# Optimization experiments

Measured on AMD Instinct MI355X. Metric: run time of the kernel, lower is better.

The kernel has to match this reference:

```python
import jax, jax.numpy as jnp
import numpy as np

B, N, D = 16, 2048, 4        # batch, input points, input feature dim (x,y,e1,e2)
G = 45                        # folding grid side -> M = G*G = 2025 output points
M = G * G
CW = 512                      # codeword dim
H1, H2 = 64, 128              # encoder hidden dims
FH = 512                      # folding MLP hidden dim


def _glorot(key, shape):
    fan_in, fan_out = shape[0], shape[1]
    s = jnp.sqrt(2.0 / (fan_in + fan_out)).astype(jnp.float32)
    return jax.random.normal(key, shape, dtype=jnp.float32) * s


def setup_inputs() -> dict:
    key = jax.random.key(0)
    ks = jax.random.split(key, 16)
    inp = {
        "points": jax.random.normal(ks[0], (B, N, D), dtype=jnp.float32),
        # encoder shared MLP: D -> H1 -> H2 -> CW, max-pool over N
        "ew1": _glorot(ks[1], (D, H1)),  "eb1": jnp.zeros((H1,), jnp.float32),
        "ew2": _glorot(ks[2], (H1, H2)), "eb2": jnp.zeros((H2,), jnp.float32),
        "ew3": _glorot(ks[3], (H2, CW)), "eb3": jnp.zeros((CW,), jnp.float32),
        # folding decoder
        "f1w1": _glorot(ks[4], (CW + 2, FH)), "f1b1": jnp.zeros((FH,), jnp.float32),
        "f1w2": _glorot(ks[5], (FH, FH)),     "f1b2": jnp.zeros((FH,), jnp.float32),
        "f1w3": _glorot(ks[6], (FH, 3)),      "f1b3": jnp.zeros((3,), jnp.float32),
        "f2w1": _glorot(ks[7], (CW + 3, FH)), "f2b1": jnp.zeros((FH,), jnp.float32),
        "f2w2": _glorot(ks[8], (FH, FH)),     "f2b2": jnp.zeros((FH,), jnp.float32),
        "f2w3": _glorot(ks[9], (FH, 3)),      "f2b3": jnp.zeros((3,), jnp.float32),
    }
    # fixed 2D folding grid in [-0.3, 0.3]^2, (M, 2)
    lin = jnp.linspace(-0.3, 0.3, G, dtype=jnp.float32)
    gx, gy = jnp.meshgrid(lin, lin, indexing="ij")
    inp["grid"] = jnp.stack([gx.ravel(), gy.ravel()], axis=-1)
    return inp


def _encode(points, ew1, eb1, ew2, eb2, ew3, eb3):
    h = jax.nn.relu(points @ ew1 + eb1)     # (B, N, H1)
    h = jax.nn.relu(h @ ew2 + eb2)          # (B, N, H2)
    h = h @ ew3 + eb3                       # (B, N, CW)
    return jnp.max(h, axis=1)               # (B, CW) codeword theta


def _decode(theta, grid, f1w1, f1b1, f1w2, f1b2, f1w3, f1b3,
            f2w1, f2b1, f2w2, f2b2, f2w3, f2b3):
    th = jnp.broadcast_to(theta[:, None, :], (theta.shape[0], M, CW))
    g = jnp.broadcast_to(grid[None], (theta.shape[0], M, 2))
    # folding 1: (codeword, 2D grid) -> 3D
    x = jnp.concatenate([th, g], axis=-1)
    x = jax.nn.relu(x @ f1w1 + f1b1)
    x = jax.nn.relu(x @ f1w2 + f1b2)
    fold1 = x @ f1w3 + f1b3                 # (B, M, 3)
    # folding 2: (codeword, intermediate 3D) -> 3D
    x = jnp.concatenate([th, fold1], axis=-1)
    x = jax.nn.relu(x @ f2w1 + f2b1)
    x = jax.nn.relu(x @ f2w2 + f2b2)
    return x @ f2w3 + f2b3                  # (B, M, 3)


def _chamfer(a, b):
    # a: (B, N, 3), b: (B, M, 3); squared-distance chamfer, both directions
    a2 = jnp.sum(a * a, axis=-1)                          # (B, N)
    b2 = jnp.sum(b * b, axis=-1)                          # (B, M)
    ab = jnp.einsum("bnd,bmd->bnm", a, b)                  # (B, N, M)
    d2 = a2[:, :, None] + b2[:, None, :] - 2.0 * ab
    d2 = jnp.maximum(d2, 0.0)
    return jnp.mean(jnp.min(d2, axis=2)) + jnp.mean(jnp.min(d2, axis=1))


def reference(points, ew1, eb1, ew2, eb2, ew3, eb3, grid,
              f1w1, f1b1, f1w2, f1b2, f1w3, f1b3,
              f2w1, f2b1, f2w2, f2b2, f2w3, f2b3):
    theta = _encode(points, ew1, eb1, ew2, eb2, ew3, eb3)
    pc_out = _decode(theta, grid, f1w1, f1b1, f1w2, f1b2, f1w3, f1b3,
                     f2w1, f2b1, f2w2, f2b2, f2w3, f2b3)
    # pc_input: (x, y, sum of energy channels)  -> (B, N, 3)
    energy = jnp.sum(points[:, :, 2:], axis=-1, keepdims=True)
    pc_input = jnp.concatenate([points[:, :, :2], energy], axis=-1)
    loss = _chamfer(pc_input, pc_out)
    return theta, pc_out, loss
```

## Files before the change

kernel.cpp:

```cpp
#include <hip/hip_runtime.h>

#define NBATCH 16
#define NPTS   2048
#define MQ     2025
#define CWDIM  512
#define NROWS  32400

typedef __attribute__((ext_vector_type(8))) short bf16x8;
typedef __attribute__((ext_vector_type(4))) float f32x4;

__device__ __forceinline__ unsigned fkey(float f) {
  unsigned u = __float_as_uint(f);
  return (u & 0x80000000u) ? ~u : (u | 0x80000000u);
}
__device__ __forceinline__ float funkey(unsigned u) {
  unsigned v = (u & 0x80000000u) ? (u ^ 0x80000000u) : ~u;
  return __uint_as_float(v);
}
__device__ __forceinline__ unsigned short f2bf(float f) {
  unsigned u = __float_as_uint(f);
  u = (u + 0x7FFFu + ((u >> 16) & 1u)) >> 16;
  return (unsigned short)u;
}

__global__ __launch_bounds__(256) void tconv_kernel(
    const float* __restrict__ ew2, unsigned short* __restrict__ ew2T)
{
  __shared__ float tile[32][33];
  const int tidx = blockIdx.x;
  const int kt = tidx >> 2, nt = tidx & 3;
  const int tx = threadIdx.x & 31, ty = threadIdx.x >> 5;
  #pragma unroll
  for (int j = 0; j < 4; ++j)
    tile[ty + 8 * j][tx] = ew2[(size_t)(kt * 32 + ty + 8 * j) * 128 + nt * 32 + tx];
  __syncthreads();
  #pragma unroll
  for (int j = 0; j < 4; ++j)
    ew2T[(size_t)(nt * 32 + ty + 8 * j) * 64 + kt * 32 + tx] = f2bf(tile[tx][ty + 8 * j]);
}

__global__ __launch_bounds__(256) void w2chunk_kernel(
    const float* __restrict__ f1w2, const float* __restrict__ f2w2,
    unsigned short* __restrict__ w2C)
{
  const int gid = blockIdx.x * 256 + threadIdx.x;
  const int s = gid >> 15;
  const int rem = gid & 32767;
  const int c16 = rem & 15, hi = (rem >> 4) & 3, cblk = (rem >> 6) & 31, kt = rem >> 11;
  const int col = cblk * 16 + c16;
  const float* src = s ? f2w2 : f1w2;
  unsigned short tmp[8];
  #pragma unroll
  for (int j = 0; j < 8; ++j)
    tmp[j] = f2bf(src[(size_t)(kt * 32 + hi * 8 + j) * 512 + col]);
  int4 pk;
  pk.x = (int)((unsigned)tmp[0] | ((unsigned)tmp[1] << 16));
  pk.y = (int)((unsigned)tmp[2] | ((unsigned)tmp[3] << 16));
  pk.z = (int)((unsigned)tmp[4] | ((unsigned)tmp[5] << 16));
  pk.w = (int)((unsigned)tmp[6] | ((unsigned)tmp[7] << 16));
  *(int4*)&w2C[(size_t)s * 262144 + (size_t)rem * 8] = pk;
}

__global__ __launch_bounds__(256) void ew3chunk_kernel(
    const float* __restrict__ ew3, unsigned short* __restrict__ ew3C)
{
  const int gid = blockIdx.x * 256 + threadIdx.x;
  const int c16 = gid & 15, hi = (gid >> 4) & 3, cblk = (gid >> 6) & 31, kblk = gid >> 11;
  const int col = cblk * 16 + c16;
  unsigned short tmp[8];
  #pragma unroll
  for (int j = 0; j < 8; ++j)
    tmp[j] = f2bf(ew3[(size_t)(kblk * 32 + hi * 8 + j) * 512 + col]);
  int4 pk;
  pk.x = (int)((unsigned)tmp[0] | ((unsigned)tmp[1] << 16));
  pk.y = (int)((unsigned)tmp[2] | ((unsigned)tmp[3] << 16));
  pk.z = (int)((unsigned)tmp[4] | ((unsigned)tmp[5] << 16));
  pk.w = (int)((unsigned)tmp[6] | ((unsigned)tmp[7] << 16));
  *(int4*)&ew3C[(size_t)gid * 8] = pk;
}

__global__ __launch_bounds__(512, 2) void enc2_kernel(
    const float* __restrict__ pts,
    const float* __restrict__ ew1, const float* __restrict__ eb1,
    const unsigned short* __restrict__ ew2T, const float* __restrict__ eb2,
    const unsigned short* __restrict__ ew3C, const float* __restrict__ eb3,
    unsigned* __restrict__ keys)
{
  __shared__ unsigned short h1s[64 * 64];
  __shared__ unsigned short h2s[64 * 128];
  __shared__ float s_pts[64][4];
  const int t = threadIdx.x;
  const int b = blockIdx.x >> 5, p0 = (blockIdx.x & 31) << 6;
  if (t < 64)
    *(float4*)&s_pts[t][0] = *(const float4*)(pts + ((size_t)b * NPTS + p0 + t) * 4);
  __syncthreads();

  {
    const int c = t & 63;
    const float w0 = ew1[c], w1 = ew1[64 + c], w2 = ew1[128 + c], w3 = ew1[192 + c];
    const float bb = eb1[c];
    #pragma unroll
    for (int i = 0; i < 8; ++i) {
      const int p = i * 8 + (t >> 6);
      float acc = bb + s_pts[p][0] * w0 + s_pts[p][1] * w1 + s_pts[p][2] * w2 + s_pts[p][3] * w3;
      unsigned byte = ((unsigned)p << 7) + ((unsigned)c << 1);
      byte ^= ((unsigned)(p & 7)) << 4;
      h1s[byte >> 1] = f2bf(fmaxf(acc, 0.f));
    }
  }
  __syncthreads();

  const int wv = t >> 6, lane = t & 63, l15 = lane & 15, hi = lane >> 4;

  {
    f32x4 acc[4];
    #pragma unroll
    for (int m = 0; m < 4; ++m) acc[m] = (f32x4){0.f, 0.f, 0.f, 0.f};
    const int col = 16 * wv + l15;
    #pragma unroll
    for (int kk = 0; kk < 64; kk += 32) {
      bf16x8 bv = *(const bf16x8*)(ew2T + (size_t)col * 64 + kk + hi * 8);
      #pragma unroll
      for (int m = 0; m < 4; ++m) {
        const int row = 16 * m + l15;
        unsigned byte = ((unsigned)row << 7) + ((unsigned)((kk + hi * 8)) << 1);
        byte ^= ((unsigned)(row & 7)) << 4;
        bf16x8 av = *(const bf16x8*)&h1s[byte >> 1];
        acc[m] = __builtin_amdgcn_mfma_f32_16x16x32_bf16(av, bv, acc[m], 0, 0, 0);
      }
    }
    const float b2c = eb2[col];
    #pragma unroll
    for (int m = 0; m < 4; ++m)
      #pragma unroll
      for (int r = 0; r < 4; ++r) {
        const int row = 16 * m + hi * 4 + r;
        unsigned byte = ((unsigned)row << 8) + ((unsigned)col << 1);
        byte ^= ((unsigned)(row & 7)) << 4;
        h2s[byte >> 1] = f2bf(fmaxf(acc[m][r] + b2c, 0.f));
      }
  }
  __syncthreads();

  {
    f32x4 acc[4][4];
    #pragma unroll
    for (int m = 0; m < 4; ++m)
      #pragma unroll
      for (int n = 0; n < 4; ++n) acc[m][n] = (f32x4){0.f, 0.f, 0.f, 0.f};
    #pragma unroll
    for (int kk = 0; kk < 128; kk += 32) {
      bf16x8 av[4];
      #pragma unroll
      for (int m = 0; m < 4; ++m) {
        const int row = 16 * m + l15;
        unsigned byte = ((unsigned)row << 8) + ((unsigned)(kk + hi * 8) << 1);
        byte ^= ((unsigned)(row & 7)) << 4;
        av[m] = *(const bf16x8*)&h2s[byte >> 1];
      }
      #pragma unroll
      for (int n = 0; n < 4; ++n) {
        bf16x8 bv = *(const bf16x8*)(ew3C +
            (size_t)(((kk >> 5) * 32 + 4 * wv + n) * 512) + lane * 8);
        #pragma unroll
        for (int m = 0; m < 4; ++m)
          acc[m][n] = __builtin_amdgcn_mfma_f32_16x16x32_bf16(av[m], bv, acc[m][n], 0, 0, 0);
      }
    }
    #pragma unroll
    for (int n = 0; n < 4; ++n) {
      const int col = 64 * wv + 16 * n + l15;
      float mx = -1e30f;
      #pragma unroll
      for (int m = 0; m < 4; ++m)
        #pragma unroll
        for (int r = 0; r < 4; ++r) mx = fmaxf(mx, acc[m][n][r]);
      mx = fmaxf(mx, __shfl_xor(mx, 16));
      mx = fmaxf(mx, __shfl_xor(mx, 32));
      if (hi == 0) atomicMax(&keys[b * CWDIM + col], fkey(mx + eb3[col]));
    }
  }
}

__global__ __launch_bounds__(256) void decode_kernel(const unsigned* __restrict__ keys,
                                                     float* __restrict__ theta) {
  int i = blockIdx.x * 256 + threadIdx.x;
  theta[i] = funkey(keys[i]);
}

__global__ __launch_bounds__(256) void h1base_kernel(
    const float* __restrict__ theta,
    const float* __restrict__ f1w1, const float* __restrict__ f1b1,
    const float* __restrict__ f2w1, const float* __restrict__ f2b1,
    float* __restrict__ h1b)
{
  int gid = blockIdx.x * 256 + threadIdx.x;
  int half = gid >> 14;
  int rem = gid & 16383;
  int stage = rem >> 13, bb = (rem >> 9) & 15, c = rem & 511;
  const float* w = stage ? f2w1 : f1w1;
  float acc = 0.f;
  if (half == 0) acc = stage ? f2b1[c] : f1b1[c];
  const float* th = theta + bb * 512 + half * 256;
  const float* wp = w + (size_t)(half * 256) * 512 + c;
  #pragma unroll 8
  for (int k = 0; k < 256; ++k) acc += th[k] * wp[(size_t)k * 512];
  atomicAdd(&h1b[rem], acc);
}

struct Fold5Smem {
  unsigned short sA[64 * 512];
  float red[8][32][3];
  float ext[64][4];
  int   rowbb[64];
};

template <int ST>
__device__ __forceinline__ void fold5_stage(Fold5Smem& S, int t, int r0,
    const float* __restrict__ h1bg,
    const float* __restrict__ w1,
    const unsigned short* __restrict__ wst,
    const float* __restrict__ b2, const float* __restrict__ w3,
    const float* __restrict__ b3, float* __restrict__ out_pc)
{
  constexpr int NE = ST ? 3 : 2;
  const int wv = t >> 6, lane = t & 63, l15 = lane & 15, hi = lane >> 4;
  const int wm = wv >> 2, wn = wv & 3;

  __syncthreads();

  {
    const int row = t & 63;
    const int bb = S.rowbb[row];
    const float e0 = S.ext[row][0], e1 = S.ext[row][1];
    float e2 = 0.f;
    if (NE == 3) e2 = S.ext[row][2];
    const float* hb  = h1bg + ST * 8192 + bb * 512;
    const float* wr0 = w1 + (size_t)512 * 512;
    const float* wr1 = wr0 + 512;
    const float* wr2 = wr1 + 512;
    #pragma unroll
    for (int i = 0; i < 8; ++i) {
      const int ko = (t >> 6) * 8 + i;
      const int c0 = ko * 8;
      float v[8];
      #pragma unroll
      for (int hf = 0; hf < 2; ++hf) {
        float4 h = *(const float4*)(hb + c0 + hf * 4);
        float4 a = *(const float4*)(wr0 + c0 + hf * 4);
        float4 bq = *(const float4*)(wr1 + c0 + hf * 4);
        v[hf * 4 + 0] = h.x + e0 * a.x + e1 * bq.x;
        v[hf * 4 + 1] = h.y + e0 * a.y + e1 * bq.y;
        v[hf * 4 + 2] = h.z + e0 * a.z + e1 * bq.z;
        v[hf * 4 + 3] = h.w + e0 * a.w + e1 * bq.w;
        if (NE == 3) {
          float4 cq = *(const float4*)(wr2 + c0 + hf * 4);
          v[hf * 4 + 0] += e2 * cq.x; v[hf * 4 + 1] += e2 * cq.y;
          v[hf * 4 + 2] += e2 * cq.z; v[hf * 4 + 3] += e2 * cq.w;
        }
      }
      int4 pk;
      pk.x = (int)((unsigned)f2bf(fmaxf(v[0], 0.f)) | ((unsigned)f2bf(fmaxf(v[1], 0.f)) << 16));
      pk.y = (int)((unsigned)f2bf(fmaxf(v[2], 0.f)) | ((unsigned)f2bf(fmaxf(v[3], 0.f)) << 16));
      pk.z = (int)((unsigned)f2bf(fmaxf(v[4], 0.f)) | ((unsigned)f2bf(fmaxf(v[5], 0.f)) << 16));
      pk.w = (int)((unsigned)f2bf(fmaxf(v[6], 0.f)) | ((unsigned)f2bf(fmaxf(v[7], 0.f)) << 16));
      *(int4*)&S.sA[(unsigned)(((ko >> 2) * 4 + (row >> 4)) * 512 + (ko & 3) * 128 + (row & 15) * 8)] = pk;
    }
  }
  __syncthreads();

  float p[2][4][3];
  #pragma unroll
  for (int m = 0; m < 2; ++m)
    #pragma unroll
    for (int r = 0; r < 4; ++r)
      #pragma unroll
      for (int jj = 0; jj < 3; ++jj) p[m][r][jj] = 0.f;

  #pragma unroll 1
  for (int pass = 0; pass < 2; ++pass) {
    f32x4 acc[2][4];
    #pragma unroll
    for (int m = 0; m < 2; ++m)
      #pragma unroll
      for (int n = 0; n < 4; ++n) acc[m][n] = (f32x4){0.f, 0.f, 0.f, 0.f};

    const unsigned short* wb = wst + (size_t)(pass * 16 + wn * 4) * 512 + lane * 8;

    #pragma unroll 2
    for (int kt = 0; kt < 16; ++kt) {
      bf16x8 bv[4];
      #pragma unroll
      for (int n = 0; n < 4; ++n)
        bv[n] = *(const bf16x8*)(wb + (size_t)(kt * 32 + n) * 512);
      const unsigned abase = (unsigned)(kt * 4 + 2 * wm) * 512 + (unsigned)lane * 8;
      bf16x8 a0 = *(const bf16x8*)&S.sA[abase];
      bf16x8 a1 = *(const bf16x8*)&S.sA[abase + 512];
      #pragma unroll
      for (int n = 0; n < 4; ++n) {
        acc[0][n] = __builtin_amdgcn_mfma_f32_16x16x32_bf16(a0, bv[n], acc[0][n], 0, 0, 0);
        acc[1][n] = __builtin_amdgcn_mfma_f32_16x16x32_bf16(a1, bv[n], acc[1][n], 0, 0, 0);
      }
    }

    #pragma unroll
    for (int n = 0; n < 4; ++n) {
      const int colG = pass * 256 + wn * 64 + 16 * n + l15;
      const float b2c = b2[colG];
      const float w30 = w3[colG * 3 + 0], w31 = w3[colG * 3 + 1], w32 = w3[colG * 3 + 2];
      #pragma unroll
      for (int m = 0; m < 2; ++m)
        #pragma unroll
        for (int r = 0; r < 4; ++r) {
          const float h = fmaxf(acc[m][n][r] + b2c, 0.f);
          p[m][r][0] += h * w30; p[m][r][1] += h * w31; p[m][r][2] += h * w32;
        }
    }
  }

  #pragma unroll
  for (int m = 0; m < 2; ++m)
    #pragma unroll
    for (int r = 0; r < 4; ++r)
      #pragma unroll
      for (int jj = 0; jj < 3; ++jj) {
        float v = p[m][r][jj];
        v += __shfl_xor(v, 1); v += __shfl_xor(v, 2);
        v += __shfl_xor(v, 4); v += __shfl_xor(v, 8);
        p[m][r][jj] = v;
      }
  if (l15 == 0) {
    #pragma unroll
    for (int m = 0; m < 2; ++m)
      #pragma unroll
      for (int r = 0; r < 4; ++r) {
        const int rl = 16 * m + hi * 4 + r;
        S.red[wv][rl][0] = p[m][r][0];
        S.red[wv][rl][1] = p[m][r][1];
        S.red[wv][rl][2] = p[m][r][2];
      }
  }
  __syncthreads();

  if (t < 192) {
    const int row = t / 3, jj = t - (t / 3) * 3;
    const int wg = (row >> 5) * 4, rl = row & 31;
    float v = b3[jj] + S.red[wg][rl][jj] + S.red[wg + 1][rl][jj]
                     + S.red[wg + 2][rl][jj] + S.red[wg + 3][rl][jj];
    if (ST == 0) S.ext[row][jj] = v;
    else if (r0 + row < NROWS) out_pc[(size_t)(r0 + row) * 3 + jj] = v;
  }
  __syncthreads();
}

__global__ __launch_bounds__(512, 2) void fold5_kernel(
    const float* __restrict__ grid2, const float* __restrict__ h1b,
    const unsigned short* __restrict__ w2C,
    const float* __restrict__ f1w1, const float* __restrict__ f1b2,
    const float* __restrict__ f1w3, const float* __restrict__ f1b3,
    const float* __restrict__ f2w1, const float* __restrict__ f2b2,
    const float* __restrict__ f2w3, const float* __restrict__ f2b3,
    float* __restrict__ out_pc)
{
  __shared__ Fold5Smem S;
  const int t = threadIdx.x;
  const int r0 = blockIdx.x * 64;

  if (t < 64) {
    const int r = r0 + t;
    const int bb = min(r / MQ, NBATCH - 1);
    S.rowbb[t] = bb;
    const int m = min(r - bb * MQ, MQ - 1);
    S.ext[t][0] = grid2[m * 2 + 0];
    S.ext[t][1] = grid2[m * 2 + 1];
    S.ext[t][2] = 0.f;
    S.ext[t][3] = 0.f;
  }

  fold5_stage<0>(S, t, r0, h1b, f1w1, w2C,          f1b2, f1w3, f1b3, nullptr);
  fold5_stage<1>(S, t, r0, h1b, f2w1, w2C + 262144, f2b2, f2w3, f2b3, out_pc);
}

__global__ __launch_bounds__(256) void chamA_kernel(const float* __restrict__ pts,
                                                    const float* __restrict__ pc,
                                                    float* __restrict__ lacc)
{
  __shared__ float sbx[2048], sby[2048], sbz[2048];
  const int t = threadIdx.x;
  const int b = blockIdx.x >> 5;
  const int n0 = (blockIdx.x & 31) << 6;
  const float* pcb = pc + (size_t)b * (MQ * 3);
  for (int i = t; i < MQ * 3; i += 256) {
    float v = pcb[i];
    int m = i / 3, j = i - m * 3;
    if (j == 0) sbx[m] = v; else if (j == 1) sby[m] = v; else sbz[m] = v;
  }
  for (int i = MQ + t; i < 2048; i += 256) { sbx[i] = 1e30f; sby[i] = 1e30f; sbz[i] = 1e30f; }
  __syncthreads();

  const int pid = t >> 4, q = t & 15;
  float ax[4], ay[4], az[4], mn[4];
  #pragma unroll
  for (int j = 0; j < 4; ++j) {
    const int n = n0 + pid * 4 + j;
    float4 P = *(const float4*)(pts + ((size_t)b * NPTS + n) * 4);
    ax[j] = P.x; ay[j] = P.y; az[j] = P.z + P.w; mn[j] = 1e30f;
  }
  #pragma unroll 4
  for (int i = 0; i < 32; ++i) {
    const int m4 = q * 4 + i * 64;
    float4 bx = *(const float4*)&sbx[m4];
    float4 by = *(const float4*)&sby[m4];
    float4 bz = *(const float4*)&sbz[m4];
    #pragma unroll
    for (int j = 0; j < 4; ++j) {
      float d0, dx, dy, dz;
      dx = ax[j] - bx.x; dy = ay[j] - by.x; dz = az[j] - bz.x; d0 = dx*dx + dy*dy + dz*dz; mn[j] = fminf(mn[j], d0);
      dx = ax[j] - bx.y; dy = ay[j] - by.y; dz = az[j] - bz.y; d0 = dx*dx + dy*dy + dz*dz; mn[j] = fminf(mn[j], d0);
      dx = ax[j] - bx.z; dy = ay[j] - by.z; dz = az[j] - bz.z; d0 = dx*dx + dy*dy + dz*dz; mn[j] = fminf(mn[j], d0);
      dx = ax[j] - bx.w; dy = ay[j] - by.w; dz = az[j] - bz.w; d0 = dx*dx + dy*dy + dz*dz; mn[j] = fminf(mn[j], d0);
    }
  }
  #pragma unroll
  for (int j = 0; j < 4; ++j) {
    mn[j] = fminf(mn[j], __shfl_xor(mn[j], 1));
    mn[j] = fminf(mn[j], __shfl_xor(mn[j], 2));
    mn[j] = fminf(mn[j], __shfl_xor(mn[j], 4));
    mn[j] = fminf(mn[j], __shfl_xor(mn[j], 8));
  }
  float v = (q == 0) ? (mn[0] + mn[1] + mn[2] + mn[3]) : 0.f;
  v += __shfl_xor(v, 16); v += __shfl_xor(v, 32);
  if ((t & 63) == 0) atomicAdd(lacc, v);
}

__global__ __launch_bounds__(256) void chamB_kernel(const float* __restrict__ pts,
                                                    const float* __restrict__ pc,
                                                    float* __restrict__ lacc)
{
  __shared__ float sax[2048], say[2048], saz[2048];
  const int t = threadIdx.x;
  const int b = blockIdx.x >> 5;
  const int m0 = (blockIdx.x & 31) << 6;
  for (int i = t; i < NPTS; i += 256) {
    float4 pp = *(const float4*)(pts + ((size_t)b * NPTS + i) * 4);
    sax[i] = pp.x; say[i] = pp.y; saz[i] = pp.z + pp.w;
  }
  __syncthreads();

  const int pid = t >> 4, q = t & 15;
  float bx[4], by[4], bz[4], mn[4];
  bool vld[4];
  #pragma unroll
  for (int j = 0; j < 4; ++j) {
    const int m = m0 + pid * 4 + j;
    vld[j] = (m < MQ);
    const int mc = vld[j] ? m : (MQ - 1);
    bx[j] = pc[(size_t)b * (MQ * 3) + mc * 3 + 0];
    by[j] = pc[(size_t)b * (MQ * 3) + mc * 3 + 1];
    bz[j] = pc[(size_t)b * (MQ * 3) + mc * 3 + 2];
    mn[j] = 1e30f;
  }
  #pragma unroll 4
  for (int i = 0; i < 32; ++i) {
    const int n4 = q * 4 + i * 64;
    float4 axv = *(const float4*)&sax[n4];
    float4 ayv = *(const float4*)&say[n4];
    float4 azv = *(const float4*)&saz[n4];
    #pragma unroll
    for (int j = 0; j < 4; ++j) {
      float d0, dx, dy, dz;
      dx = axv.x - bx[j]; dy = ayv.x - by[j]; dz = azv.x - bz[j]; d0 = dx*dx + dy*dy + dz*dz; mn[j] = fminf(mn[j], d0);
      dx = axv.y - bx[j]; dy = ayv.y - by[j]; dz = azv.y - bz[j]; d0 = dx*dx + dy*dy + dz*dz; mn[j] = fminf(mn[j], d0);
      dx = axv.z - bx[j]; dy = ayv.z - by[j]; dz = azv.z - bz[j]; d0 = dx*dx + dy*dy + dz*dz; mn[j] = fminf(mn[j], d0);
      dx = axv.w - bx[j]; dy = ayv.w - by[j]; dz = azv.w - bz[j]; d0 = dx*dx + dy*dy + dz*dz; mn[j] = fminf(mn[j], d0);
    }
  }
  #pragma unroll
  for (int j = 0; j < 4; ++j) {
    mn[j] = fminf(mn[j], __shfl_xor(mn[j], 1));
    mn[j] = fminf(mn[j], __shfl_xor(mn[j], 2));
    mn[j] = fminf(mn[j], __shfl_xor(mn[j], 4));
    mn[j] = fminf(mn[j], __shfl_xor(mn[j], 8));
  }
  float v = 0.f;
  if (q == 0) {
    #pragma unroll
    for (int j = 0; j < 4; ++j) if (vld[j]) v += mn[j];
  }
  v += __shfl_xor(v, 16); v += __shfl_xor(v, 32);
  if ((t & 63) == 0) atomicAdd(lacc + 1, v);
}

__global__ void fin_kernel(const float* __restrict__ lacc, float* __restrict__ loss) {
  if (threadIdx.x == 0 && blockIdx.x == 0)
    loss[0] = lacc[0] * (1.0f / (NBATCH * NPTS)) + lacc[1] * (1.0f / (NBATCH * MQ));
}

extern "C" void kernel_launch(void* const* d_in, const int* in_sizes, int n_in,
                              void* d_out, int out_size, void* d_ws, size_t ws_size,
                              hipStream_t stream) {
  const float* pts  = (const float*)d_in[0];
  const float* ew1  = (const float*)d_in[1];
  const float* eb1  = (const float*)d_in[2];
  const float* ew2  = (const float*)d_in[3];
  const float* eb2  = (const float*)d_in[4];
  const float* ew3  = (const float*)d_in[5];
  const float* eb3  = (const float*)d_in[6];
  const float* f1w1 = (const float*)d_in[7];
  const float* f1b1 = (const float*)d_in[8];
  const float* f1w2 = (const float*)d_in[9];
  const float* f1b2 = (const float*)d_in[10];
  const float* f1w3 = (const float*)d_in[11];
  const float* f1b3 = (const float*)d_in[12];
  const float* f2w1 = (const float*)d_in[13];
  const float* f2b1 = (const float*)d_in[14];
  const float* f2w2 = (const float*)d_in[15];
  const float* f2b2 = (const float*)d_in[16];
  const float* f2w3 = (const float*)d_in[17];
  const float* f2b3 = (const float*)d_in[18];
  const float* grid2= (const float*)d_in[19];

  float* out = (float*)d_out;
  unsigned* keys       = (unsigned*)d_ws;
  float* lacc          = (float*)((char*)d_ws + 32768);
  float* h1b           = (float*)((char*)d_ws + 33024);
  unsigned short* w2C  = (unsigned short*)((char*)d_ws + 98560);
  unsigned short* ew2T = (unsigned short*)((char*)d_ws + 1147136);
  unsigned short* ew3C = (unsigned short*)((char*)d_ws + 1163520);

  hipMemsetAsync(d_ws, 0, 98560, stream);

  tconv_kernel<<<8, 256, 0, stream>>>(ew2, ew2T);
  w2chunk_kernel<<<256, 256, 0, stream>>>(f1w2, f2w2, w2C);
  ew3chunk_kernel<<<32, 256, 0, stream>>>(ew3, ew3C);
  enc2_kernel<<<512, 512, 0, stream>>>(pts, ew1, eb1, ew2T, eb2, ew3C, eb3, keys);
  decode_kernel<<<32, 256, 0, stream>>>(keys, out);
  h1base_kernel<<<128, 256, 0, stream>>>(out, f1w1, f1b1, f2w1, f2b1, h1b);
  fold5_kernel<<<507, 512, 0, stream>>>(grid2, h1b, w2C,
                                        f1w1, f1b2, f1w3, f1b3,
                                        f2w1, f2b2, f2w3, f2b3,
                                        out + 8192);
  chamA_kernel<<<512, 256, 0, stream>>>(pts, out + 8192, lacc);
  chamB_kernel<<<512, 256, 0, stream>>>(pts, out + 8192, lacc);
  fin_kernel<<<1, 64, 0, stream>>>(lacc, out + 8192 + 97200);
}
```

Baseline: 269.5 us.

## Merge prep kernels, fold decode into h1base, fuse chamfer passes with finalize

Merges three weight-conversion kernels and the workspace memset into one prep kernel. Folds the key-to-theta decode into h1base, which now stages theta in shared memory. Merges both chamfer directions into one 1024-block launch that writes the final loss through a last-block-done counter. Wraps the MFMA burst in fold5 with s_setprio. The aim is fewer launches and less inter-kernel gap overhead, at the cost of branchy multi-role kernels and a grid-wide atomic counter.

```diff
diff --git a/kernel.cpp b/kernel.cpp
--- a/kernel.cpp
+++ b/kernel.cpp
@@ -23,60 +23,61 @@
   return (unsigned short)u;
 }
 
-__global__ __launch_bounds__(256) void tconv_kernel(
-    const float* __restrict__ ew2, unsigned short* __restrict__ ew2T)
+__global__ __launch_bounds__(256) void prep_kernel(
+    const float* __restrict__ ew2, const float* __restrict__ ew3,
+    const float* __restrict__ f1w2, const float* __restrict__ f2w2,
+    unsigned short* __restrict__ ew2T, unsigned short* __restrict__ ew3C,
+    unsigned short* __restrict__ w2C, unsigned* __restrict__ zws)
 {
   __shared__ float tile[32][33];
-  const int tidx = blockIdx.x;
-  const int kt = tidx >> 2, nt = tidx & 3;
-  const int tx = threadIdx.x & 31, ty = threadIdx.x >> 5;
-  #pragma unroll
-  for (int j = 0; j < 4; ++j)
-    tile[ty + 8 * j][tx] = ew2[(size_t)(kt * 32 + ty + 8 * j) * 128 + nt * 32 + tx];
-  __syncthreads();
-  #pragma unroll
-  for (int j = 0; j < 4; ++j)
-    ew2T[(size_t)(nt * 32 + ty + 8 * j) * 64 + kt * 32 + tx] = f2bf(tile[tx][ty + 8 * j]);
-}
-
-__global__ __launch_bounds__(256) void w2chunk_kernel(
-    const float* __restrict__ f1w2, const float* __restrict__ f2w2,
-    unsigned short* __restrict__ w2C)
-{
-  const int gid = blockIdx.x * 256 + threadIdx.x;
-  const int s = gid >> 15;
-  const int rem = gid & 32767;
-  const int c16 = rem & 15, hi = (rem >> 4) & 3, cblk = (rem >> 6) & 31, kt = rem >> 11;
-  const int col = cblk * 16 + c16;
-  const float* src = s ? f2w2 : f1w2;
-  unsigned short tmp[8];
-  #pragma unroll
-  for (int j = 0; j < 8; ++j)
-    tmp[j] = f2bf(src[(size_t)(kt * 32 + hi * 8 + j) * 512 + col]);
-  int4 pk;
-  pk.x = (int)((unsigned)tmp[0] | ((unsigned)tmp[1] << 16));
-  pk.y = (int)((unsigned)tmp[2] | ((unsigned)tmp[3] << 16));
-  pk.z = (int)((unsigned)tmp[4] | ((unsigned)tmp[5] << 16));
-  pk.w = (int)((unsigned)tmp[6] | ((unsigned)tmp[7] << 16));
-  *(int4*)&w2C[(size_t)s * 262144 + (size_t)rem * 8] = pk;
-}
-
-__global__ __launch_bounds__(256) void ew3chunk_kernel(
-    const float* __restrict__ ew3, unsigned short* __restrict__ ew3C)
-{
-  const int gid = blockIdx.x * 256 + threadIdx.x;
-  const int c16 = gid & 15, hi = (gid >> 4) & 3, cblk = (gid >> 6) & 31, kblk = gid >> 11;
-  const int col = cblk * 16 + c16;
-  unsigned short tmp[8];
-  #pragma unroll
-  for (int j = 0; j < 8; ++j)
-    tmp[j] = f2bf(ew3[(size_t)(kblk * 32 + hi * 8 + j) * 512 + col]);
-  int4 pk;
-  pk.x = (int)((unsigned)tmp[0] | ((unsigned)tmp[1] << 16));
-  pk.y = (int)((unsigned)tmp[2] | ((unsigned)tmp[3] << 16));
-  pk.z = (int)((unsigned)tmp[4] | ((unsigned)tmp[5] << 16));
-  pk.w = (int)((unsigned)tmp[6] | ((unsigned)tmp[7] << 16));
-  *(int4*)&ew3C[(size_t)gid * 8] = pk;
+  const int blk = blockIdx.x;
+  const int t = threadIdx.x;
+
+  if (blk < 8) {
+    const int kt = blk >> 2, nt = blk & 3;
+    const int tx = t & 31, ty = t >> 5;
+    #pragma unroll
+    for (int j = 0; j < 4; ++j)
+      tile[ty + 8 * j][tx] = ew2[(size_t)(kt * 32 + ty + 8 * j) * 128 + nt * 32 + tx];
+    __syncthreads();
+    #pragma unroll
+    for (int j = 0; j < 4; ++j)
+      ew2T[(size_t)(nt * 32 + ty + 8 * j) * 64 + kt * 32 + tx] = f2bf(tile[tx][ty + 8 * j]);
+  } else if (blk < 40) {
+    const int gid = (blk - 8) * 256 + t;
+    const int c16 = gid & 15, hi = (gid >> 4) & 3, cblk = (gid >> 6) & 31, kblk = gid >> 11;
+    const int col = cblk * 16 + c16;
+    unsigned short tmp[8];
+    #pragma unroll
+    for (int j = 0; j < 8; ++j)
+      tmp[j] = f2bf(ew3[(size_t)(kblk * 32 + hi * 8 + j) * 512 + col]);
+    int4 pk;
+    pk.x = (int)((unsigned)tmp[0] | ((unsigned)tmp[1] << 16));
+    pk.y = (int)((unsigned)tmp[2] | ((unsigned)tmp[3] << 16));
+    pk.z = (int)((unsigned)tmp[4] | ((unsigned)tmp[5] << 16));
+    pk.w = (int)((unsigned)tmp[6] | ((unsigned)tmp[7] << 16));
+    *(int4*)&ew3C[(size_t)gid * 8] = pk;
+  } else if (blk < 296) {
+    const int gid = (blk - 40) * 256 + t;
+    const int s = gid >> 15;
+    const int rem = gid & 32767;
+    const int c16 = rem & 15, hi = (rem >> 4) & 3, cblk = (rem >> 6) & 31, kt = rem >> 11;
+    const int col = cblk * 16 + c16;
+    const float* src = s ? f2w2 : f1w2;
+    unsigned short tmp[8];
+    #pragma unroll
+    for (int j = 0; j < 8; ++j)
+      tmp[j] = f2bf(src[(size_t)(kt * 32 + hi * 8 + j) * 512 + col]);
+    int4 pk;
+    pk.x = (int)((unsigned)tmp[0] | ((unsigned)tmp[1] << 16));
+    pk.y = (int)((unsigned)tmp[2] | ((unsigned)tmp[3] << 16));
+    pk.z = (int)((unsigned)tmp[4] | ((unsigned)tmp[5] << 16));
+    pk.w = (int)((unsigned)tmp[6] | ((unsigned)tmp[7] << 16));
+    *(int4*)&w2C[(size_t)s * 262144 + (size_t)rem * 8] = pk;
+  } else {
+    const int idx = (blk - 296) * 256 + t;
+    for (int i = idx; i < 24640; i += 6144) zws[i] = 0u;
+  }
 }
 
 __global__ __launch_bounds__(512, 2) void enc2_kernel(
@@ -182,29 +183,26 @@
   }
 }
 
-__global__ __launch_bounds__(256) void decode_kernel(const unsigned* __restrict__ keys,
-                                                     float* __restrict__ theta) {
-  int i = blockIdx.x * 256 + threadIdx.x;
-  theta[i] = funkey(keys[i]);
-}
-
 __global__ __launch_bounds__(256) void h1base_kernel(
-    const float* __restrict__ theta,
+    const unsigned* __restrict__ keys, float* __restrict__ theta_out,
     const float* __restrict__ f1w1, const float* __restrict__ f1b1,
     const float* __restrict__ f2w1, const float* __restrict__ f2b1,
     float* __restrict__ h1b)
 {
-  int gid = blockIdx.x * 256 + threadIdx.x;
-  int half = gid >> 14;
-  int rem = gid & 16383;
-  int stage = rem >> 13, bb = (rem >> 9) & 15, c = rem & 511;
+  __shared__ float thl[256];
+  const int t = threadIdx.x;
+  const int gid = blockIdx.x * 256 + t;
+  const int half = gid >> 14;
+  const int rem = gid & 16383;
+  const int stage = rem >> 13, bb = (rem >> 9) & 15, c = rem & 511;
+  thl[t] = funkey(keys[bb * 512 + half * 256 + t]);
+  if (gid < 8192) theta_out[gid] = funkey(keys[gid]);
+  __syncthreads();
   const float* w = stage ? f2w1 : f1w1;
-  float acc = 0.f;
-  if (half == 0) acc = stage ? f2b1[c] : f1b1[c];
-  const float* th = theta + bb * 512 + half * 256;
+  float acc = (half == 0) ? (stage ? f2b1[c] : f1b1[c]) : 0.f;
   const float* wp = w + (size_t)(half * 256) * 512 + c;
   #pragma unroll 8
-  for (int k = 0; k < 256; ++k) acc += th[k] * wp[(size_t)k * 512];
+  for (int k = 0; k < 256; ++k) acc += thl[k] * wp[(size_t)k * 512];
   atomicAdd(&h1b[rem], acc);
 }
 
@@ -296,11 +294,13 @@
       const unsigned abase = (unsigned)(kt * 4 + 2 * wm) * 512 + (unsigned)lane * 8;
       bf16x8 a0 = *(const bf16x8*)&S.sA[abase];
       bf16x8 a1 = *(const bf16x8*)&S.sA[abase + 512];
+      __builtin_amdgcn_s_setprio(1);
       #pragma unroll
       for (int n = 0; n < 4; ++n) {
         acc[0][n] = __builtin_amdgcn_mfma_f32_16x16x32_bf16(a0, bv[n], acc[0][n], 0, 0, 0);
         acc[1][n] = __builtin_amdgcn_mfma_f32_16x16x32_bf16(a1, bv[n], acc[1][n], 0, 0, 0);
       }
+      __builtin_amdgcn_s_setprio(0);
     }
 
     #pragma unroll
@@ -381,119 +381,122 @@
   fold5_stage<1>(S, t, r0, h1b, f2w1, w2C + 262144, f2b2, f2w3, f2b3, out_pc);
 }
 
-__global__ __launch_bounds__(256) void chamA_kernel(const float* __restrict__ pts,
-                                                    const float* __restrict__ pc,
-                                                    float* __restrict__ lacc)
+__global__ __launch_bounds__(256) void cham_kernel(
+    const float* __restrict__ pts, const float* __restrict__ pc,
+    float* __restrict__ lacc, float* __restrict__ loss)
 {
-  __shared__ float sbx[2048], sby[2048], sbz[2048];
+  __shared__ float s0[2048], s1[2048], s2[2048];
   const int t = threadIdx.x;
-  const int b = blockIdx.x >> 5;
-  const int n0 = (blockIdx.x & 31) << 6;
-  const float* pcb = pc + (size_t)b * (MQ * 3);
-  for (int i = t; i < MQ * 3; i += 256) {
-    float v = pcb[i];
-    int m = i / 3, j = i - m * 3;
-    if (j == 0) sbx[m] = v; else if (j == 1) sby[m] = v; else sbz[m] = v;
-  }
-  for (int i = MQ + t; i < 2048; i += 256) { sbx[i] = 1e30f; sby[i] = 1e30f; sbz[i] = 1e30f; }
-  __syncthreads();
-
-  const int pid = t >> 4, q = t & 15;
-  float ax[4], ay[4], az[4], mn[4];
-  #pragma unroll
-  for (int j = 0; j < 4; ++j) {
-    const int n = n0 + pid * 4 + j;
-    float4 P = *(const float4*)(pts + ((size_t)b * NPTS + n) * 4);
-    ax[j] = P.x; ay[j] = P.y; az[j] = P.z + P.w; mn[j] = 1e30f;
-  }
-  #pragma unroll 4
-  for (int i = 0; i < 32; ++i) {
-    const int m4 = q * 4 + i * 64;
-    float4 bx = *(const float4*)&sbx[m4];
-    float4 by = *(const float4*)&sby[m4];
-    float4 bz = *(const float4*)&sbz[m4];
+  const int side = blockIdx.x >> 9;
+  const int ib = blockIdx.x & 511;
+  const int b = ib >> 5;
+
+  if (side == 0) {
+    const int n0 = (ib & 31) << 6;
+    const float* pcb = pc + (size_t)b * (MQ * 3);
+    for (int i = t; i < MQ * 3; i += 256) {
+      float v = pcb[i];
+      int m = i / 3, j = i - m * 3;
+      if (j == 0) s0[m] = v; else if (j == 1) s1[m] = v; else s2[m] = v;
+    }
+    for (int i = MQ + t; i < 2048; i += 256) { s0[i] = 1e30f; s1[i] = 1e30f; s2[i] = 1e30f; }
+    __syncthreads();
+
+    const int pid = t >> 4, q = t & 15;
+    float ax[4], ay[4], az[4], mn[4];
     #pragma unroll
     for (int j = 0; j < 4; ++j) {
-      float d0, dx, dy, dz;
-      dx = ax[j] - bx.x; dy = ay[j] - by.x; dz = az[j] - bz.x; d0 = dx*dx + dy*dy + dz*dz; mn[j] = fminf(mn[j], d0);
-      dx = ax[j] - bx.y; dy = ay[j] - by.y; dz = az[j] - bz.y; d0 = dx*dx + dy*dy + dz*dz; mn[j] = fminf(mn[j], d0);
-      dx = ax[j] - bx.z; dy = ay[j] - by.z; dz = az[j] - bz.z; d0 = dx*dx + dy*dy + dz*dz; mn[j] = fminf(mn[j], d0);
-      dx = ax[j] - bx.w; dy = ay[j] - by.w; dz = az[j] - bz.w; d0 = dx*dx + dy*dy + dz*dz; mn[j] = fminf(mn[j], d0);
-    }
-  }
-  #pragma unroll
-  for (int j = 0; j < 4; ++j) {
-    mn[j] = fminf(mn[j], __shfl_xor(mn[j], 1));
-    mn[j] = fminf(mn[j], __shfl_xor(mn[j], 2));
-    mn[j] = fminf(mn[j], __shfl_xor(mn[j], 4));
-    mn[j] = fminf(mn[j], __shfl_xor(mn[j], 8));
-  }
-  float v = (q == 0) ? (mn[0] + mn[1] + mn[2] + mn[3]) : 0.f;
-  v += __shfl_xor(v, 16); v += __shfl_xor(v, 32);
-  if ((t & 63) == 0) atomicAdd(lacc, v);
-}
-
-__global__ __launch_bounds__(256) void chamB_kernel(const float* __restrict__ pts,
-                                                    const float* __restrict__ pc,
-                                                    float* __restrict__ lacc)
-{
-  __shared__ float sax[2048], say[2048], saz[2048];
-  const int t = threadIdx.x;
-  const int b = blockIdx.x >> 5;
-  const int m0 = (blockIdx.x & 31) << 6;
-  for (int i = t; i < NPTS; i += 256) {
-    float4 pp = *(const float4*)(pts + ((size_t)b * NPTS + i) * 4);
-    sax[i] = pp.x; say[i] = pp.y; saz[i] = pp.z + pp.w;
-  }
-  __syncthreads();
-
-  const int pid = t >> 4, q = t & 15;
-  float bx[4], by[4], bz[4], mn[4];
-  bool vld[4];
-  #pragma unroll
-  for (int j = 0; j < 4; ++j) {
-    const int m = m0 + pid * 4 + j;
-    vld[j] = (m < MQ);
-    const int mc = vld[j] ? m : (MQ - 1);
-    bx[j] = pc[(size_t)b * (MQ * 3) + mc * 3 + 0];
-    by[j] = pc[(size_t)b * (MQ * 3) + mc * 3 + 1];
-    bz[j] = pc[(size_t)b * (MQ * 3) + mc * 3 + 2];
-    mn[j] = 1e30f;
-  }
-  #pragma unroll 4
-  for (int i = 0; i < 32; ++i) {
-    const int n4 = q * 4 + i * 64;
-    float4 axv = *(const float4*)&sax[n4];
-    float4 ayv = *(const float4*)&say[n4];
-    float4 azv = *(const float4*)&saz[n4];
+      const int n = n0 + pid * 4 + j;
+      float4 P = *(const float4*)(pts + ((size_t)b * NPTS + n) * 4);
+      ax[j] = P.x; ay[j] = P.y; az[j] = P.z + P.w; mn[j] = 1e30f;
+    }
+    #pragma unroll 4
+    for (int i = 0; i < 32; ++i) {
+      const int m4 = q * 4 + i * 64;
+      float4 bx = *(const float4*)&s0[m4];
+      float4 by = *(const float4*)&s1[m4];
+      float4 bz = *(const float4*)&s2[m4];
+      #pragma unroll
+      for (int j = 0; j < 4; ++j) {
+        float d0, dx, dy, dz;
+        dx = ax[j] - bx.x; dy = ay[j] - by.x; dz = az[j] - bz.x; d0 = dx*dx + dy*dy + dz*dz; mn[j] = fminf(mn[j], d0);
+        dx = ax[j] - bx.y; dy = ay[j] - by.y; dz = az[j] - bz.y; d0 = dx*dx + dy*dy + dz*dz; mn[j] = fminf(mn[j], d0);
+        dx = ax[j] - bx.z; dy = ay[j] - by.z; dz = az[j] - bz.z; d0 = dx*dx + dy*dy + dz*dz; mn[j] = fminf(mn[j], d0);
+        dx = ax[j] - bx.w; dy = ay[j] - by.w; dz = az[j] - bz.w; d0 = dx*dx + dy*dy + dz*dz; mn[j] = fminf(mn[j], d0);
+      }
+    }
     #pragma unroll
     for (int j = 0; j < 4; ++j) {
-      float d0, dx, dy, dz;
-      dx = axv.x - bx[j]; dy = ayv.x - by[j]; dz = azv.x - bz[j]; d0 = dx*dx + dy*dy + dz*dz; mn[j] = fminf(mn[j], d0);
-      dx = axv.y - bx[j]; dy = ayv.y - by[j]; dz = azv.y - bz[j]; d0 = dx*dx + dy*dy + dz*dz; mn[j] = fminf(mn[j], d0);
-      dx = axv.z - bx[j]; dy = ayv.z - by[j]; dz = azv.z - bz[j]; d0 = dx*dx + dy*dy + dz*dz; mn[j] = fminf(mn[j], d0);
-      dx = axv.w - bx[j]; dy = ayv.w - by[j]; dz = azv.w - bz[j]; d0 = dx*dx + dy*dy + dz*dz; mn[j] = fminf(mn[j], d0);
-    }
-  }
-  #pragma unroll
-  for (int j = 0; j < 4; ++j) {
-    mn[j] = fminf(mn[j], __shfl_xor(mn[j], 1));
-    mn[j] = fminf(mn[j], __shfl_xor(mn[j], 2));
-    mn[j] = fminf(mn[j], __shfl_xor(mn[j], 4));
-    mn[j] = fminf(mn[j], __shfl_xor(mn[j], 8));
-  }
-  float v = 0.f;
-  if (q == 0) {
-    #pragma unroll
-    for (int j = 0; j < 4; ++j) if (vld[j]) v += mn[j];
-  }
-  v += __shfl_xor(v, 16); v += __shfl_xor(v, 32);
-  if ((t & 63) == 0) atomicAdd(lacc + 1, v);
-}
-
-__global__ void fin_kernel(const float* __restrict__ lacc, float* __restrict__ loss) {
-  if (threadIdx.x == 0 && blockIdx.x == 0)
-    loss[0] = lacc[0] * (1.0f / (NBATCH * NPTS)) + lacc[1] * (1.0f / (NBATCH * MQ));
+      mn[j] = fminf(mn[j], __shfl_xor(mn[j], 1));
+      mn[j] = fminf(mn[j], __shfl_xor(mn[j], 2));
+      mn[j] = fminf(mn[j], __shfl_xor(mn[j], 4));
+      mn[j] = fminf(mn[j], __shfl_xor(mn[j], 8));
+    }
+    float v = (q == 0) ? (mn[0] + mn[1] + mn[2] + mn[3]) : 0.f;
+    v += __shfl_xor(v, 16); v += __shfl_xor(v, 32);
+    if ((t & 63) == 0) atomicAdd(lacc, v);
+  } else {
+    const int m0 = (ib & 31) << 6;
+    for (int i = t; i < NPTS; i += 256) {
+      float4 pp = *(const float4*)(pts + ((size_t)b * NPTS + i) * 4);
+      s0[i] = pp.x; s1[i] = pp.y; s2[i] = pp.z + pp.w;
+    }
+    __syncthreads();
+
+    const int pid = t >> 4, q = t & 15;
+    float bx[4], by[4], bz[4], mn[4];
+    bool vld[4];
+    #pragma unroll
+    for (int j = 0; j < 4; ++j) {
+      const int m = m0 + pid * 4 + j;
+      vld[j] = (m < MQ);
+      const int mc = vld[j] ? m : (MQ - 1);
+      bx[j] = pc[(size_t)b * (MQ * 3) + mc * 3 + 0];
+      by[j] = pc[(size_t)b * (MQ * 3) + mc * 3 + 1];
+      bz[j] = pc[(size_t)b * (MQ * 3) + mc * 3 + 2];
+      mn[j] = 1e30f;
+    }
+    #pragma unroll 4
+    for (int i = 0; i < 32; ++i) {
+      const int n4 = q * 4 + i * 64;
+      float4 axv = *(const float4*)&s0[n4];
+      float4 ayv = *(const float4*)&s1[n4];
+      float4 azv = *(const float4*)&s2[n4];
+      #pragma unroll
+      for (int j = 0; j < 4; ++j) {
+        float d0, dx, dy, dz;
+        dx = axv.x - bx[j]; dy = ayv.x - by[j]; dz = azv.x - bz[j]; d0 = dx*dx + dy*dy + dz*dz; mn[j] = fminf(mn[j], d0);
+        dx = axv.y - bx[j]; dy = ayv.y - by[j]; dz = azv.y - bz[j]; d0 = dx*dx + dy*dy + dz*dz; mn[j] = fminf(mn[j], d0);
+        dx = axv.z - bx[j]; dy = ayv.z - by[j]; dz = azv.z - bz[j]; d0 = dx*dx + dy*dy + dz*dz; mn[j] = fminf(mn[j], d0);
+        dx = axv.w - bx[j]; dy = ayv.w - by[j]; dz = azv.w - bz[j]; d0 = dx*dx + dy*dy + dz*dz; mn[j] = fminf(mn[j], d0);
+      }
+    }
+    #pragma unroll
+    for (int j = 0; j < 4; ++j) {
+      mn[j] = fminf(mn[j], __shfl_xor(mn[j], 1));
+      mn[j] = fminf(mn[j], __shfl_xor(mn[j], 2));
+      mn[j] = fminf(mn[j], __shfl_xor(mn[j], 4));
+      mn[j] = fminf(mn[j], __shfl_xor(mn[j], 8));
+    }
+    float v = 0.f;
+    if (q == 0) {
+      #pragma unroll
+      for (int j = 0; j < 4; ++j) if (vld[j]) v += mn[j];
+    }
+    v += __shfl_xor(v, 16); v += __shfl_xor(v, 32);
+    if ((t & 63) == 0) atomicAdd(lacc + 1, v);
+  }
+
+  __syncthreads();
+  if (t == 0) {
+    __threadfence();
+    unsigned old = atomicAdd((unsigned*)(lacc + 2), 1u);
+    if (old == 1023u) {
+      float l0 = atomicAdd(lacc, 0.f);
+      float l1 = atomicAdd(lacc + 1, 0.f);
+      loss[0] = l0 * (1.0f / (NBATCH * NPTS)) + l1 * (1.0f / (NBATCH * MQ));
+    }
+  }
 }
 
 extern "C" void kernel_launch(void* const* d_in, const int* in_sizes, int n_in,
@@ -528,19 +531,14 @@
   unsigned short* ew2T = (unsigned short*)((char*)d_ws + 1147136);
   unsigned short* ew3C = (unsigned short*)((char*)d_ws + 1163520);
 
-  hipMemsetAsync(d_ws, 0, 98560, stream);
-
-  tconv_kernel<<<8, 256, 0, stream>>>(ew2, ew2T);
-  w2chunk_kernel<<<256, 256, 0, stream>>>(f1w2, f2w2, w2C);
-  ew3chunk_kernel<<<32, 256, 0, stream>>>(ew3, ew3C);
+  prep_kernel<<<320, 256, 0, stream>>>(ew2, ew3, f1w2, f2w2,
+                                       ew2T, ew3C, w2C, (unsigned*)d_ws);
   enc2_kernel<<<512, 512, 0, stream>>>(pts, ew1, eb1, ew2T, eb2, ew3C, eb3, keys);
-  decode_kernel<<<32, 256, 0, stream>>>(keys, out);
-  h1base_kernel<<<128, 256, 0, stream>>>(out, f1w1, f1b1, f2w1, f2b1, h1b);
+  h1base_kernel<<<128, 256, 0, stream>>>(keys, out, f1w1, f1b1, f2w1, f2b1, h1b);
   fold5_kernel<<<507, 512, 0, stream>>>(grid2, h1b, w2C,
                                         f1w1, f1b2, f1w3, f1b3,
                                         f2w1, f2b2, f2w3, f2b3,
                                         out + 8192);
-  chamA_kernel<<<512, 256, 0, stream>>>(pts, out + 8192, lacc);
-  chamB_kernel<<<512, 256, 0, stream>>>(pts, out + 8192, lacc);
-  fin_kernel<<<1, 64, 0, stream>>>(lacc, out + 8192 + 97200);
-}
+  cham_kernel<<<1024, 256, 0, stream>>>(pts, out + 8192, lacc,
+                                        out + 8192 + 97200);
+}
```

Result: faster. 253.4 us (-6.0%).
